# Kernel tuning notes

Hardware: AMD Instinct MI355X
Metric: run time of the kernel (lower is better)

The kernel has to match this reference:

```python
import jax, jax.numpy as jnp
import numpy as np

B, N, M, F1, F2 = 8, 128, 256, 256, 256


def setup_inputs() -> dict:
    key = jax.random.key(0)
    k = jax.random.split(key, 6)
    s = 1.0 / np.sqrt(F1)
    return {
        "x": jax.random.normal(k[0], (B, N, F1), dtype=jnp.float32),
        "y": jax.random.normal(k[1], (B, M, F2), dtype=jnp.float32),
        "U_w": jax.random.normal(k[2], (F2, F1), dtype=jnp.float32) * s,
        "U_b": jax.random.normal(k[3], (F2,), dtype=jnp.float32) * s,
        "W_w": jax.random.normal(k[4], (1, F2), dtype=jnp.float32) * (1.0 / np.sqrt(F2)),
        "W_b": jax.random.normal(k[5], (1,), dtype=jnp.float32) * (1.0 / np.sqrt(F2)),
    }


def reference(x, y, U_w, U_b, W_w, W_b):
    # poolAttn path (default). dropout=0 -> identity.
    u = jnp.einsum('bnf,gf->bng', x, U_w) + U_b          # [B,N,F2]
    # broadcast bilinear: tanh(u[:,:,None,:] * y[:,None,:,:]) -> [B,N,M,F2]
    a = jnp.tanh(u[:, :, None, :] * y[:, None, :, :])
    alpha = jnp.einsum('bnmf,f->bnm', a, W_w[0]) + W_b[0]  # [B,N,M]
    # x attention: max over M, softmax over N
    xw = jax.nn.softmax(alpha.max(axis=2), axis=1)         # [B,N]
    x_pooled = jnp.einsum('bnf,bn->bf', x, xw)             # [B,F1]
    # y attention: max over N, softmax over M
    yw = jax.nn.softmax(alpha.max(axis=1), axis=1)         # [B,M]
    y_pooled = jnp.einsum('bm,bmf->bf', yw, y)             # [B,F2]
    return jnp.concatenate([x_pooled, y_pooled], axis=1)   # [B,F1+F2]
```

## Files before the change

kernel.cpp:

```cpp
#include <hip/hip_runtime.h>
#include <math.h>

#define B_ 8
#define N_ 128
#define M_ 256
#define F_ 256

#define LOG2E2 2.8853900817779268f

__global__ __launch_bounds__(256) void k1_lite(const float* __restrict__ x,
                                               const float* __restrict__ Uw,
                                               const float* __restrict__ Ub,
                                               float* __restrict__ u) {
  const int g  = threadIdx.x;
  const int r0 = blockIdx.x * 4;
  const float* __restrict__ uwr = Uw + (size_t)g * F_;
  const float* __restrict__ xr  = x + (size_t)r0 * F_;

  float a0 = 0.f, a1 = 0.f, a2 = 0.f, a3 = 0.f;
#pragma unroll 4
  for (int f = 0; f < F_; f += 4) {
    const float4 wv = *(const float4*)&uwr[f];
    const float4 x0 = *(const float4*)&xr[0 * F_ + f];
    const float4 x1 = *(const float4*)&xr[1 * F_ + f];
    const float4 x2 = *(const float4*)&xr[2 * F_ + f];
    const float4 x3 = *(const float4*)&xr[3 * F_ + f];
    a0 = fmaf(wv.x, x0.x, a0); a0 = fmaf(wv.y, x0.y, a0);
    a0 = fmaf(wv.z, x0.z, a0); a0 = fmaf(wv.w, x0.w, a0);
    a1 = fmaf(wv.x, x1.x, a1); a1 = fmaf(wv.y, x1.y, a1);
    a1 = fmaf(wv.z, x1.z, a1); a1 = fmaf(wv.w, x1.w, a1);
    a2 = fmaf(wv.x, x2.x, a2); a2 = fmaf(wv.y, x2.y, a2);
    a2 = fmaf(wv.z, x2.z, a2); a2 = fmaf(wv.w, x2.w, a2);
    a3 = fmaf(wv.x, x3.x, a3); a3 = fmaf(wv.y, x3.y, a3);
    a3 = fmaf(wv.z, x3.z, a3); a3 = fmaf(wv.w, x3.w, a3);
  }
  const float ubv = Ub[g];
  u[(size_t)(r0 + 0) * F_ + g] = (a0 + ubv) * LOG2E2;
  u[(size_t)(r0 + 1) * F_ + g] = (a1 + ubv) * LOG2E2;
  u[(size_t)(r0 + 2) * F_ + g] = (a2 + ubv) * LOG2E2;
  u[(size_t)(r0 + 3) * F_ + g] = (a3 + ubv) * LOG2E2;
}

__global__ void k2_alpha(const float* __restrict__ u,
                         const float* __restrict__ y,
                         const float* __restrict__ Ww,
                         float* __restrict__ rminp,
                         float* __restrict__ cminp) {
  __shared__ float us[8][F_];
  __shared__ float ys[64][132];
  __shared__ float red[8][8][64];
  __shared__ float sm[8][64];

  const int tid  = threadIdx.x;
  const int mg   = blockIdx.x;
  const int ns   = blockIdx.y;
  const int b    = blockIdx.z;
  const int n0   = ns * 8;
  const int m0   = mg * 64;
  const int lane = tid & 63;
  const int w    = tid >> 6;
  const int fc   = __builtin_amdgcn_readfirstlane(w);

  {
    const int r = tid >> 6, c = (tid & 63) * 4;
    *(float4*)&us[r][c] =
        *(const float4*)&u[(size_t)(b * N_ + n0 + r) * F_ + c];
  }
  float4 wwv[8];
  {
    const float* wr = Ww + fc * 32;
#pragma unroll
    for (int j = 0; j < 8; ++j) wwv[j] = *(const float4*)&wr[4 * j];
  }

  float4 yv[8];
  const float* __restrict__ ybase = y + (size_t)(b * M_ + m0) * F_;
#pragma unroll
  for (int k = 0; k < 4; ++k) {
    const int flat = tid + k * 512;
    const int row = flat >> 5, col = (flat & 31) * 4;
    *(float4*)&ys[row][col] = *(const float4*)&ybase[(size_t)row * F_ + col];
  }
  __syncthreads();
  if (w < 4) {
    const int base = fc * 32;
#pragma unroll
    for (int j = 0; j < 8; ++j) yv[j] = *(const float4*)&ys[lane][base + 4 * j];
  }
  __syncthreads();
#pragma unroll
  for (int k = 0; k < 4; ++k) {
    const int flat = tid + k * 512;
    const int row = flat >> 5, col = (flat & 31) * 4;
    *(float4*)&ys[row][col] =
        *(const float4*)&ybase[(size_t)row * F_ + 128 + col];
  }
  __syncthreads();
  if (w >= 4) {
    const int base = (fc - 4) * 32;
#pragma unroll
    for (int j = 0; j < 8; ++j) yv[j] = *(const float4*)&ys[lane][base + 4 * j];
  }
  __syncthreads();

#define QUAD(nn, j, S0, S1)                                                              \
  do {                                                                                   \
    const float4 uv = *(const float4*)&us[nn][fc * 32 + 4 * (j)];                        \
    S0 = fmaf(wwv[j].x,                                                                  \
              __builtin_amdgcn_rcpf(__builtin_amdgcn_exp2f(uv.x * yv[j].x) + 1.f), S0);  \
    S1 = fmaf(wwv[j].y,                                                                  \
              __builtin_amdgcn_rcpf(__builtin_amdgcn_exp2f(uv.y * yv[j].y) + 1.f), S1);  \
    S0 = fmaf(wwv[j].z,                                                                  \
              __builtin_amdgcn_rcpf(__builtin_amdgcn_exp2f(uv.z * yv[j].z) + 1.f), S0);  \
    S1 = fmaf(wwv[j].w,                                                                  \
              __builtin_amdgcn_rcpf(__builtin_amdgcn_exp2f(uv.w * yv[j].w) + 1.f), S1);  \
  } while (0)

#define DO_N(nn, A)                                                                      \
  do {                                                                                   \
    float s0 = 0.f, s1 = 0.f;                                                            \
    QUAD(nn, 0, s0, s1); QUAD(nn, 1, s0, s1); QUAD(nn, 2, s0, s1); QUAD(nn, 3, s0, s1);  \
    QUAD(nn, 4, s0, s1); QUAD(nn, 5, s0, s1); QUAD(nn, 6, s0, s1); QUAD(nn, 7, s0, s1);  \
    A = s0 + s1;                                                                         \
  } while (0)

  float a0, a1, a2, a3, a4, a5, a6, a7;
  DO_N(0, a0); DO_N(1, a1); DO_N(2, a2); DO_N(3, a3);
  DO_N(4, a4); DO_N(5, a5); DO_N(6, a6); DO_N(7, a7);
#undef DO_N
#undef QUAD

  red[0][fc][lane] = a0; red[1][fc][lane] = a1;
  red[2][fc][lane] = a2; red[3][fc][lane] = a3;
  red[4][fc][lane] = a4; red[5][fc][lane] = a5;
  red[6][fc][lane] = a6; red[7][fc][lane] = a7;
  __syncthreads();

  float S = 0.f;
#pragma unroll
  for (int k = 0; k < 8; ++k) S += red[w][k][lane];

  float r = S;
#pragma unroll
  for (int s = 32; s; s >>= 1) r = fminf(r, __shfl_xor(r, s));
  if (lane == 0) rminp[((size_t)b * 4 + mg) * N_ + n0 + w] = r;

  sm[w][lane] = S;
  __syncthreads();
  if (w == 0) {
    float c = sm[0][lane];
#pragma unroll
    for (int k = 1; k < 8; ++k) c = fminf(c, sm[k][lane]);
    cminp[((size_t)b * 16 + ns) * M_ + m0 + lane] = c;
  }
}

__global__ __launch_bounds__(256) void kb_final(
    const float* __restrict__ x, const float* __restrict__ y,
    const float* __restrict__ rminp, const float* __restrict__ cminp,
    float* __restrict__ out) {
  const int b    = blockIdx.x;
  const int task = blockIdx.y;
  const int fq   = blockIdx.z;
  const int tid  = threadIdx.x;
  const int w    = tid >> 6;
  __shared__ float wgt[M_];
  __shared__ float redv[4];
  __shared__ float part[4][64];

  if (task == 0) {
    float rv = -INFINITY;
    if (tid < N_) {
      float v = INFINITY;
#pragma unroll
      for (int mg = 0; mg < 4; ++mg)
        v = fminf(v, rminp[((size_t)b * 4 + mg) * N_ + tid]);
      rv = -2.f * v;
    }
    float m1 = rv;
#pragma unroll
    for (int s = 32; s; s >>= 1) m1 = fmaxf(m1, __shfl_xor(m1, s));
    if ((tid & 63) == 0) redv[w] = m1;
    __syncthreads();
    m1 = fmaxf(fmaxf(redv[0], redv[1]), fmaxf(redv[2], redv[3]));
    __syncthreads();
    const float e1 = (tid < N_) ? __expf(rv - m1) : 0.f;
    float s1 = e1;
#pragma unroll
    for (int s = 32; s; s >>= 1) s1 += __shfl_xor(s1, s);
    if ((tid & 63) == 0) redv[w] = s1;
    __syncthreads();
    s1 = redv[0] + redv[1] + redv[2] + redv[3];
    if (tid < N_) wgt[tid] = e1 / s1;
    __syncthreads();

    const int f = fq * 64 + (tid & 63);
    const int q = w;
    float acc = 0.f;
#pragma unroll 8
    for (int n = q; n < N_; n += 4)
      acc = fmaf(wgt[n], x[(size_t)(b * N_ + n) * F_ + f], acc);
    part[q][tid & 63] = acc;
    __syncthreads();
    if (tid < 64)
      out[b * (2 * F_) + fq * 64 + tid] =
          part[0][tid] + part[1][tid] + part[2][tid] + part[3][tid];
  } else {
    float cv;
    {
      float c = INFINITY;
#pragma unroll
      for (int ns = 0; ns < 16; ++ns)
        c = fminf(c, cminp[((size_t)b * 16 + ns) * M_ + tid]);
      cv = -2.f * c;
    }
    float m2 = cv;
#pragma unroll
    for (int s = 32; s; s >>= 1) m2 = fmaxf(m2, __shfl_xor(m2, s));
    if ((tid & 63) == 0) redv[w] = m2;
    __syncthreads();
    m2 = fmaxf(fmaxf(redv[0], redv[1]), fmaxf(redv[2], redv[3]));
    __syncthreads();
    const float e2 = __expf(cv - m2);
    float s2 = e2;
#pragma unroll
    for (int s = 32; s; s >>= 1) s2 += __shfl_xor(s2, s);
    if ((tid & 63) == 0) redv[w] = s2;
    __syncthreads();
    s2 = redv[0] + redv[1] + redv[2] + redv[3];
    wgt[tid] = e2 / s2;
    __syncthreads();

    const int f = fq * 64 + (tid & 63);
    const int q = w;
    float acc = 0.f;
#pragma unroll 8
    for (int m = q; m < M_; m += 4)
      acc = fmaf(wgt[m], y[(size_t)(b * M_ + m) * F_ + f], acc);
    part[q][tid & 63] = acc;
    __syncthreads();
    if (tid < 64)
      out[b * (2 * F_) + F_ + fq * 64 + tid] =
          part[0][tid] + part[1][tid] + part[2][tid] + part[3][tid];
  }
}

extern "C" void kernel_launch(void* const* d_in, const int* in_sizes, int n_in,
                              void* d_out, int out_size, void* d_ws, size_t ws_size,
                              hipStream_t stream) {
  (void)in_sizes; (void)n_in; (void)out_size; (void)ws_size;
  const float* x  = (const float*)d_in[0];
  const float* y  = (const float*)d_in[1];
  const float* Uw = (const float*)d_in[2];
  const float* Ub = (const float*)d_in[3];
  const float* Ww = (const float*)d_in[4];

  float* u     = (float*)d_ws;
  float* rminp = u + B_ * N_ * F_;
  float* cminp = rminp + B_ * 4 * N_;
  float* outp  = (float*)d_out;

  k1_lite<<<dim3((B_ * N_) / 4), 256, 0, stream>>>(x, Uw, Ub, u);
  k2_alpha<<<dim3(4, 16, B_), 512, 0, stream>>>(u, y, Ww, rminp, cminp);
  kb_final<<<dim3(B_, 2, 4), 256, 0, stream>>>(x, y, rminp, cminp, outp);
}
```

Measured before the change: 35.56 us.

## Halve rows per block in alpha kernel, load y directly, stage Ww in LDS

The alpha kernel now handles 4 query rows per block instead of 8, which doubles the grid to 1024 blocks and doubles the partial column-min buffer that the final kernel reduces over. The staged double-pass copy of y through shared memory, with its extra barriers, is replaced by each thread reading its own y slice straight from global memory. The Ww slice moves from registers into a shared-memory vector, and the min reductions are reorganized. The aim is higher occupancy and fewer barriers. In exchange, y is reloaded twice as often, the per-thread global reads are strided across rows, and the partial-min workspace is larger.

```diff
diff --git a/kernel.cpp b/kernel.cpp
--- a/kernel.cpp
+++ b/kernel.cpp
@@ -46,73 +46,49 @@
                          const float* __restrict__ Ww,
                          float* __restrict__ rminp,
                          float* __restrict__ cminp) {
-  __shared__ float us[8][F_];
-  __shared__ float ys[64][132];
-  __shared__ float red[8][8][64];
-  __shared__ float sm[8][64];
+  __shared__ float us[4][F_];
+  __shared__ float ww[F_];
+  __shared__ float red[4][8][64];
+  __shared__ float sm[4][64];
 
   const int tid  = threadIdx.x;
   const int mg   = blockIdx.x;
   const int ns   = blockIdx.y;
   const int b    = blockIdx.z;
-  const int n0   = ns * 8;
+  const int n0   = ns * 4;
   const int m0   = mg * 64;
   const int lane = tid & 63;
   const int w    = tid >> 6;
   const int fc   = __builtin_amdgcn_readfirstlane(w);
 
-  {
+  if (tid < 256) {
     const int r = tid >> 6, c = (tid & 63) * 4;
     *(float4*)&us[r][c] =
         *(const float4*)&u[(size_t)(b * N_ + n0 + r) * F_ + c];
-  }
-  float4 wwv[8];
+  } else if (tid < 320) {
+    const int c = (tid - 256) * 4;
+    *(float4*)&ww[c] = *(const float4*)&Ww[c];
+  }
+
+  float4 yv[8];
   {
-    const float* wr = Ww + fc * 32;
-#pragma unroll
-    for (int j = 0; j < 8; ++j) wwv[j] = *(const float4*)&wr[4 * j];
-  }
-
-  float4 yv[8];
-  const float* __restrict__ ybase = y + (size_t)(b * M_ + m0) * F_;
-#pragma unroll
-  for (int k = 0; k < 4; ++k) {
-    const int flat = tid + k * 512;
-    const int row = flat >> 5, col = (flat & 31) * 4;
-    *(float4*)&ys[row][col] = *(const float4*)&ybase[(size_t)row * F_ + col];
-  }
-  __syncthreads();
-  if (w < 4) {
-    const int base = fc * 32;
-#pragma unroll
-    for (int j = 0; j < 8; ++j) yv[j] = *(const float4*)&ys[lane][base + 4 * j];
-  }
-  __syncthreads();
-#pragma unroll
-  for (int k = 0; k < 4; ++k) {
-    const int flat = tid + k * 512;
-    const int row = flat >> 5, col = (flat & 31) * 4;
-    *(float4*)&ys[row][col] =
-        *(const float4*)&ybase[(size_t)row * F_ + 128 + col];
-  }
-  __syncthreads();
-  if (w >= 4) {
-    const int base = (fc - 4) * 32;
-#pragma unroll
-    for (int j = 0; j < 8; ++j) yv[j] = *(const float4*)&ys[lane][base + 4 * j];
+    const float* yr = y + ((size_t)(b * M_ + m0 + lane)) * F_ + fc * 32;
+#pragma unroll
+    for (int j = 0; j < 8; ++j) yv[j] = *(const float4*)&yr[4 * j];
   }
   __syncthreads();
 
 #define QUAD(nn, j, S0, S1)                                                              \
   do {                                                                                   \
-    const float4 uv = *(const float4*)&us[nn][fc * 32 + 4 * (j)];                        \
-    S0 = fmaf(wwv[j].x,                                                                  \
+    const float4 uv  = *(const float4*)&us[nn][fc * 32 + 4 * (j)];                       \
+    const float4 wv4 = *(const float4*)&ww[fc * 32 + 4 * (j)];                           \
+    S0 = fmaf(wv4.x,                                                                     \
               __builtin_amdgcn_rcpf(__builtin_amdgcn_exp2f(uv.x * yv[j].x) + 1.f), S0);  \
-    S1 = fmaf(wwv[j].y,                                                                  \
+    S1 = fmaf(wv4.y,                                                                     \
               __builtin_amdgcn_rcpf(__builtin_amdgcn_exp2f(uv.y * yv[j].y) + 1.f), S1);  \
-    S0 = fmaf(wwv[j].z,                                                                  \
+    S0 = fmaf(wv4.z,                                                                     \
               __builtin_amdgcn_rcpf(__builtin_amdgcn_exp2f(uv.z * yv[j].z) + 1.f), S0);  \
-    S1 = fmaf(wwv[j].w,                                                                  \
+    S1 = fmaf(wv4.w,                                                                     \
               __builtin_amdgcn_rcpf(__builtin_amdgcn_exp2f(uv.w * yv[j].w) + 1.f), S1);  \
   } while (0)
 
@@ -124,34 +100,34 @@
     A = s0 + s1;                                                                         \
   } while (0)
 
-  float a0, a1, a2, a3, a4, a5, a6, a7;
+  float a0, a1, a2, a3;
   DO_N(0, a0); DO_N(1, a1); DO_N(2, a2); DO_N(3, a3);
-  DO_N(4, a4); DO_N(5, a5); DO_N(6, a6); DO_N(7, a7);
 #undef DO_N
 #undef QUAD
 
   red[0][fc][lane] = a0; red[1][fc][lane] = a1;
   red[2][fc][lane] = a2; red[3][fc][lane] = a3;
-  red[4][fc][lane] = a4; red[5][fc][lane] = a5;
-  red[6][fc][lane] = a6; red[7][fc][lane] = a7;
   __syncthreads();
 
-  float S = 0.f;
-#pragma unroll
-  for (int k = 0; k < 8; ++k) S += red[w][k][lane];
-
-  float r = S;
-#pragma unroll
-  for (int s = 32; s; s >>= 1) r = fminf(r, __shfl_xor(r, s));
-  if (lane == 0) rminp[((size_t)b * 4 + mg) * N_ + n0 + w] = r;
-
-  sm[w][lane] = S;
+  if (tid < 256) {
+    const int n = tid >> 6, mm = tid & 63;
+    float S = 0.f;
+#pragma unroll
+    for (int k = 0; k < 8; ++k) S += red[n][k][mm];
+    sm[n][mm] = S;
+  }
   __syncthreads();
-  if (w == 0) {
-    float c = sm[0][lane];
-#pragma unroll
-    for (int k = 1; k < 8; ++k) c = fminf(c, sm[k][lane]);
-    cminp[((size_t)b * 16 + ns) * M_ + m0 + lane] = c;
+
+  if (w < 4) {
+    float v = sm[w][lane];
+#pragma unroll
+    for (int s = 32; s; s >>= 1) v = fminf(v, __shfl_xor(v, s));
+    if (lane == 0) rminp[((size_t)b * 4 + mg) * N_ + n0 + w] = v;
+  }
+  if (tid < 64) {
+    const float c = fminf(fminf(sm[0][tid], sm[1][tid]),
+                          fminf(sm[2][tid], sm[3][tid]));
+    cminp[((size_t)b * 32 + ns) * M_ + m0 + tid] = c;
   }
 }
 
@@ -195,12 +171,11 @@
     __syncthreads();
 
     const int f = fq * 64 + (tid & 63);
-    const int q = w;
     float acc = 0.f;
 #pragma unroll 8
-    for (int n = q; n < N_; n += 4)
+    for (int n = w; n < N_; n += 4)
       acc = fmaf(wgt[n], x[(size_t)(b * N_ + n) * F_ + f], acc);
-    part[q][tid & 63] = acc;
+    part[w][tid & 63] = acc;
     __syncthreads();
     if (tid < 64)
       out[b * (2 * F_) + fq * 64 + tid] =
@@ -210,8 +185,8 @@
     {
       float c = INFINITY;
 #pragma unroll
-      for (int ns = 0; ns < 16; ++ns)
-        c = fminf(c, cminp[((size_t)b * 16 + ns) * M_ + tid]);
+      for (int ns = 0; ns < 32; ++ns)
+        c = fminf(c, cminp[((size_t)b * 32 + ns) * M_ + tid]);
       cv = -2.f * c;
     }
     float m2 = cv;
@@ -232,12 +207,11 @@
     __syncthreads();
 
     const int f = fq * 64 + (tid & 63);
-    const int q = w;
     float acc = 0.f;
 #pragma unroll 8
-    for (int m = q; m < M_; m += 4)
+    for (int m = w; m < M_; m += 4)
       acc = fmaf(wgt[m], y[(size_t)(b * M_ + m) * F_ + f], acc);
-    part[q][tid & 63] = acc;
+    part[w][tid & 63] = acc;
     __syncthreads();
     if (tid < 64)
       out[b * (2 * F_) + F_ + fq * 64 + tid] =
@@ -261,6 +235,6 @@
   float* outp  = (float*)d_out;
 
   k1_lite<<<dim3((B_ * N_) / 4), 256, 0, stream>>>(x, Uw, Ub, u);
-  k2_alpha<<<dim3(4, 16, B_), 512, 0, stream>>>(u, y, Ww, rminp, cminp);
+  k2_alpha<<<dim3(4, 32, B_), 512, 0, stream>>>(u, y, Ww, rminp, cminp);
   kb_final<<<dim3(B_, 2, 4), 256, 0, stream>>>(x, y, rminp, cminp, outp);
 }
```

Result: no change. 35.77 us (+0.6%).

## Load y directly into registers and pair reciprocals in sigmoid-weighted sum

Applied to the files above, without the earlier changes.

Each thread now loads its y slice straight from global memory into registers, dropping the padded shared-memory staging buffer and three barriers. The inner sigmoid-weighted sum combines two terms over a common denominator, so it needs one rcp per pair of elements instead of one per element. This cuts transcendental-unit work in the hot loop and frees LDS, which may raise occupancy. In exchange the global y loads are strided per lane and less coalesced, and the product of two (1+exp2) terms can overflow to inf for large arguments, which changes rounding.

```diff
diff --git a/kernel.cpp b/kernel.cpp
--- a/kernel.cpp
+++ b/kernel.cpp
@@ -47,7 +47,6 @@
                          float* __restrict__ rminp,
                          float* __restrict__ cminp) {
   __shared__ float us[8][F_];
-  __shared__ float ys[64][132];
   __shared__ float red[8][8][64];
   __shared__ float sm[8][64];
 
@@ -66,54 +65,35 @@
     *(float4*)&us[r][c] =
         *(const float4*)&u[(size_t)(b * N_ + n0 + r) * F_ + c];
   }
+
+  float4 yv[8];
   float4 wwv[8];
   {
+    const float* yr = y + ((size_t)(b * M_ + m0 + lane)) * F_ + fc * 32;
     const float* wr = Ww + fc * 32;
 #pragma unroll
-    for (int j = 0; j < 8; ++j) wwv[j] = *(const float4*)&wr[4 * j];
-  }
-
-  float4 yv[8];
-  const float* __restrict__ ybase = y + (size_t)(b * M_ + m0) * F_;
-#pragma unroll
-  for (int k = 0; k < 4; ++k) {
-    const int flat = tid + k * 512;
-    const int row = flat >> 5, col = (flat & 31) * 4;
-    *(float4*)&ys[row][col] = *(const float4*)&ybase[(size_t)row * F_ + col];
+    for (int j = 0; j < 8; ++j) {
+      yv[j]  = *(const float4*)&yr[4 * j];
+      wwv[j] = *(const float4*)&wr[4 * j];
+    }
   }
   __syncthreads();
-  if (w < 4) {
-    const int base = fc * 32;
-#pragma unroll
-    for (int j = 0; j < 8; ++j) yv[j] = *(const float4*)&ys[lane][base + 4 * j];
-  }
-  __syncthreads();
-#pragma unroll
-  for (int k = 0; k < 4; ++k) {
-    const int flat = tid + k * 512;
-    const int row = flat >> 5, col = (flat & 31) * 4;
-    *(float4*)&ys[row][col] =
-        *(const float4*)&ybase[(size_t)row * F_ + 128 + col];
-  }
-  __syncthreads();
-  if (w >= 4) {
-    const int base = (fc - 4) * 32;
-#pragma unroll
-    for (int j = 0; j < 8; ++j) yv[j] = *(const float4*)&ys[lane][base + 4 * j];
-  }
-  __syncthreads();
-
-#define QUAD(nn, j, S0, S1)                                                              \
-  do {                                                                                   \
-    const float4 uv = *(const float4*)&us[nn][fc * 32 + 4 * (j)];                        \
-    S0 = fmaf(wwv[j].x,                                                                  \
-              __builtin_amdgcn_rcpf(__builtin_amdgcn_exp2f(uv.x * yv[j].x) + 1.f), S0);  \
-    S1 = fmaf(wwv[j].y,                                                                  \
-              __builtin_amdgcn_rcpf(__builtin_amdgcn_exp2f(uv.y * yv[j].y) + 1.f), S1);  \
-    S0 = fmaf(wwv[j].z,                                                                  \
-              __builtin_amdgcn_rcpf(__builtin_amdgcn_exp2f(uv.z * yv[j].z) + 1.f), S0);  \
-    S1 = fmaf(wwv[j].w,                                                                  \
-              __builtin_amdgcn_rcpf(__builtin_amdgcn_exp2f(uv.w * yv[j].w) + 1.f), S1);  \
+
+#define QUAD(nn, j, S0, S1)                                                   \
+  do {                                                                        \
+    const float4 uv = *(const float4*)&us[nn][fc * 32 + 4 * (j)];             \
+    const float t0 = uv.x * yv[j].x;                                          \
+    const float t1 = uv.y * yv[j].y;                                          \
+    const float t2 = uv.z * yv[j].z;                                          \
+    const float t3 = uv.w * yv[j].w;                                          \
+    const float d0 = 1.f + __builtin_amdgcn_exp2f(t0);                        \
+    const float d1 = 1.f + __builtin_amdgcn_exp2f(t1);                        \
+    const float d2 = 1.f + __builtin_amdgcn_exp2f(t2);                        \
+    const float d3 = 1.f + __builtin_amdgcn_exp2f(t3);                        \
+    const float n01 = fmaf(wwv[j].x, d1, wwv[j].y * d0);                      \
+    const float n23 = fmaf(wwv[j].z, d3, wwv[j].w * d2);                      \
+    S0 = fmaf(n01, __builtin_amdgcn_rcpf(d0 * d1), S0);                       \
+    S1 = fmaf(n23, __builtin_amdgcn_rcpf(d2 * d3), S1);                       \
   } while (0)
 
 #define DO_N(nn, A)                                                                      \
@@ -195,12 +175,11 @@
     __syncthreads();
 
     const int f = fq * 64 + (tid & 63);
-    const int q = w;
     float acc = 0.f;
 #pragma unroll 8
-    for (int n = q; n < N_; n += 4)
+    for (int n = w; n < N_; n += 4)
       acc = fmaf(wgt[n], x[(size_t)(b * N_ + n) * F_ + f], acc);
-    part[q][tid & 63] = acc;
+    part[w][tid & 63] = acc;
     __syncthreads();
     if (tid < 64)
       out[b * (2 * F_) + fq * 64 + tid] =
@@ -232,12 +211,11 @@
     __syncthreads();
 
     const int f = fq * 64 + (tid & 63);
-    const int q = w;
     float acc = 0.f;
 #pragma unroll 8
-    for (int m = q; m < M_; m += 4)
+    for (int m = w; m < M_; m += 4)
       acc = fmaf(wgt[m], y[(size_t)(b * M_ + m) * F_ + f], acc);
-    part[q][tid & 63] = acc;
+    part[w][tid & 63] = acc;
     __syncthreads();
     if (tid < 64)
       out[b * (2 * F_) + F_ + fq * 64 + tid] =
```

After: 35.05 us (median of 2 runs). Within noise of the previous version (-1.4%).
